# Kernel tuning notes

Measured on AMD Instinct MI355X. Metric: run time of the kernel, lower is better.

Reference implementation:

```python
import jax, jax.numpy as jnp
import numpy as np

B, W, K = 8, 200, 100   # batch, window_size, n_features
KS = 7                   # conv kernel size
HID = 150                # GRU hidden dim
ALPHA = 0.2              # leaky relu slope
FE = 2 * W               # feature GAT embed dim (gatv2 doubles window_size)
TE = 2 * K               # temporal GAT embed dim (gatv2 doubles n_features)


def setup_inputs() -> dict:
    key = jax.random.key(0)
    ks = jax.random.split(key, 16)
    s = lambda k, shape, sc=0.05: jax.random.normal(k, shape, jnp.float32) * sc
    return {
        "x": jax.random.normal(ks[0], (B, W, K), jnp.float32),
        "conv_w": s(ks[1], (K, K, KS)),
        "conv_b": s(ks[2], (K,)),
        "f_lin_w": s(ks[3], (2 * W, FE)),
        "f_lin_b": s(ks[4], (FE,)),
        "f_a": s(ks[5], (FE,)),
        "f_bias": s(ks[6], (K, K)),
        "t_lin_w": s(ks[7], (2 * K, TE)),
        "t_lin_b": s(ks[8], (TE,)),
        "t_a": s(ks[9], (TE,)),
        "t_bias": s(ks[10], (W, W)),
        "w_ih": s(ks[11], (3 * HID, 3 * K)),
        "w_hh": s(ks[12], (3 * HID, HID)),
        "b_ih": s(ks[13], (3 * HID,)),
        "b_hh": s(ks[14], (3 * HID,)),
    }


def _leaky(x):
    return jnp.where(x >= 0, x, ALPHA * x)


def _gatv2(v, lin_w, lin_b, a, bias):
    """GATv2 layer over fully-connected graph. v: (b, N, D).
    e_ij = a . leakyrelu(W [v_i || v_j] + b_lin); out = sigmoid(softmax(e+bias) @ v).
    Splitting W rows avoids materializing the (b,N,N,2D) concat tensor."""
    D = v.shape[-1]
    w1, w2 = lin_w[:D], lin_w[D:]
    si = jnp.einsum('bnd,de->bne', v, w1)  # contribution of node i (repeated)
    sj = jnp.einsum('bnd,de->bne', v, w2)  # contribution of node j (alternating)
    g = _leaky(si[:, :, None, :] + sj[:, None, :, :] + lin_b)  # (b,N,N,E)
    e = jnp.einsum('bije,e->bij', g, a) + bias                 # (b,N,N)
    attn = jax.nn.softmax(e, axis=2)
    return jax.nn.sigmoid(jnp.einsum('bij,bjd->bid', attn, v))  # (b,N,D)


def _forward(x, conv_w, conv_b, f_lin_w, f_lin_b, f_a, f_bias,
             t_lin_w, t_lin_b, t_a, t_bias, w_ih, w_hh, b_ih, b_hh):
    # ConvLayer: permute to (b,K,W), pad 3 both sides, conv1d k=7, relu, permute back
    xc = jnp.transpose(x, (0, 2, 1))
    xc = jax.lax.conv_general_dilated(xc, conv_w, (1,), [((KS - 1) // 2, (KS - 1) // 2)],
                                      dimension_numbers=('NCH', 'OIH', 'NCH'))
    xc = jax.nn.relu(xc + conv_b[None, :, None])
    xc = jnp.transpose(xc, (0, 2, 1))  # (b, W, K)

    # Feature GAT: nodes = features, per-node vector = window
    h_feat = _gatv2(jnp.transpose(xc, (0, 2, 1)), f_lin_w, f_lin_b, f_a, f_bias)
    h_feat = jnp.transpose(h_feat, (0, 2, 1))  # (b, W, K)
    # Temporal GAT: nodes = timesteps, per-node vector = features
    h_temp = _gatv2(xc, t_lin_w, t_lin_b, t_a, t_bias)  # (b, W, K)

    h_cat = jnp.concatenate([xc, h_feat, h_temp], axis=2)  # (b, W, 3K)

    # Single-layer GRU, torch gate order (r, z, n), batch_first; return final hidden
    def step(h, xt):
        gi = xt @ w_ih.T + b_ih
        gh = h @ w_hh.T + b_hh
        ir, iz, inn = jnp.split(gi, 3, axis=-1)
        hr, hz, hn = jnp.split(gh, 3, axis=-1)
        r = jax.nn.sigmoid(ir + hr)
        z = jax.nn.sigmoid(iz + hz)
        n = jnp.tanh(inn + r * hn)
        return (1.0 - z) * n + z * h, None

    h0 = jnp.zeros((x.shape[0], HID), x.dtype)
    h_end, _ = jax.lax.scan(step, h0, jnp.transpose(h_cat, (1, 0, 2)))
    return h_end  # (b, HID)


def reference(x, conv_w, conv_b, f_lin_w, f_lin_b, f_a, f_bias,
              t_lin_w, t_lin_b, t_a, t_bias, w_ih, w_hh, b_ih, b_hh):
    return _forward(x, conv_w, conv_b, f_lin_w, f_lin_b, f_a, f_bias,
                    t_lin_w, t_lin_b, t_a, t_bias, w_ih, w_hh, b_ih, b_hh)
```

## Files before the change

### kernel.cpp

```cpp
#include <hip/hip_runtime.h>
#include <math.h>

#define NB   8
#define NW   200
#define NK   100
#define KSZ  7
#define NHID 150
#define NFE  400
#define NTE  200
#define NG   450
#define NCIN 300
#define ALPHAC 0.2f

typedef __attribute__((ext_vector_type(8))) short bf8;
typedef __attribute__((ext_vector_type(4))) float f32x4;

__device__ __forceinline__ float sigmoidf_(float x){
  return 1.0f/(1.0f + __expf(-x));
}
__device__ __forceinline__ float tanhf_(float x){
  float xc = fminf(fmaxf(x, -15.f), 15.f);
  float e = __expf(2.f*xc);
  return (e - 1.f)/(e + 1.f);
}
__device__ __forceinline__ unsigned short f2bf(float f){
  unsigned int u = __float_as_uint(f);
  unsigned int r = u + 0x7FFFu + ((u>>16)&1u);
  return (unsigned short)(r>>16);
}
__device__ __forceinline__ float lrelu_(float x){
  return fmaxf(x, 0.f) + ALPHAC*fminf(x, 0.f);
}

__global__ void prep_kernel(const float* conv_w, const float* w_ih, const float* w_hh,
                            float* conv_wT, float* w_ihT, unsigned int* Bfrag){
  int idx = blockIdx.x*256 + threadIdx.x;
  const int n1 = NK*NK*KSZ;
  const int n2 = NG*NCIN;
  const int n3 = 32*5*64*4;
  if (idx < n1){
    int k = idx % NK; int it = idx / NK;
    int i = it / KSZ, t = it % KSZ;
    conv_wT[idx] = conv_w[(k*NK + i)*KSZ + t];
  } else if (idx < n1 + n2){
    int o = idx - n1; int g = o % NG; int c = o / NG;
    w_ihT[o] = w_ih[g*NCIN + c];
  } else if (idx < n1 + n2 + n3){
    int o = idx - n1 - n2;
    int n   = o / 1280;
    int rem = o % 1280;
    int ks  = rem / 256;
    int rem2= rem % 256;
    int l   = rem2 >> 2;
    int d   = rem2 & 3;
    int col = n*16 + (l & 15);
    int k0  = ks*32 + (l >> 4)*8 + d*2;
    unsigned short lo = 0, hi = 0;
    if (col < NG){
      if (k0     < NHID) lo = f2bf(w_hh[col*NHID + k0]);
      if (k0 + 1 < NHID) hi = f2bf(w_hh[col*NHID + k0 + 1]);
    }
    Bfrag[o] = ((unsigned int)hi << 16) | lo;
  }
}

__global__ void conv_kernel(const float* x, const float* conv_b, const float* conv_wT, float* xc){
  int idx = blockIdx.x*256 + threadIdx.x;
  if (idx >= NB*NW*NK) return;
  int k = idx % NK; int w = (idx/NK) % NW; int b = idx/(NK*NW);
  float acc = conv_b[k];
  const float* xb = x + b*NW*NK;
  for (int t = 0; t < KSZ; ++t){
    int ws = w + t - 3;
    if (ws < 0 || ws >= NW) continue;
    const float* xr = xb + ws*NK;
    const float* wr = conv_wT + t*NK + k;
    #pragma unroll 4
    for (int i = 0; i < NK; ++i){
      acc += xr[i] * wr[i*KSZ*NK];
    }
  }
  xc[idx] = fmaxf(acc, 0.0f);
}

__global__ void sisj_fused(const float* xc, const float* f_lin_w, float* si_f, float* sj_f,
                           const float* t_lin_w, float* si_t, float* sj_t){
  __shared__ __align__(16) float vt[NW*4];
  int tid = threadIdx.x;
  if (blockIdx.x < 200){
    int b = blockIdx.x / 25; int n0 = (blockIdx.x % 25)*4;
    for (int d = tid; d < NW; d += 512){
      float4 v = *(const float4*)&xc[(b*NW + d)*NK + n0];
      *(float4*)&vt[d*4] = v;
    }
    __syncthreads();
    if (tid >= NFE) return;
    int e = tid;
    float a1[4] = {0,0,0,0}, a2[4] = {0,0,0,0};
    for (int d = 0; d < NW; ++d){
      float w1 = f_lin_w[d*NFE + e];
      float w2 = f_lin_w[(NW + d)*NFE + e];
      float4 v = *(const float4*)&vt[d*4];
      a1[0] += v.x*w1; a1[1] += v.y*w1; a1[2] += v.z*w1; a1[3] += v.w*w1;
      a2[0] += v.x*w2; a2[1] += v.y*w2; a2[2] += v.z*w2; a2[3] += v.w*w2;
    }
    #pragma unroll
    for (int nn = 0; nn < 4; ++nn){
      si_f[(b*NK + n0+nn)*NFE + e] = a1[nn];
      sj_f[(b*NK + n0+nn)*NFE + e] = a2[nn];
    }
  } else {
    int bi = blockIdx.x - 200;
    int b = bi / 50; int n0 = (bi % 50)*4;
    for (int idx = tid; idx < 4*25; idx += 512){
      int nn = idx & 3; int d4 = idx >> 2;
      float4 v = *(const float4*)&xc[(b*NW + n0+nn)*NK + d4*4];
      vt[(d4*4+0)*4 + nn] = v.x;
      vt[(d4*4+1)*4 + nn] = v.y;
      vt[(d4*4+2)*4 + nn] = v.z;
      vt[(d4*4+3)*4 + nn] = v.w;
    }
    __syncthreads();
    if (tid >= NTE) return;
    int e = tid;
    float a1[4] = {0,0,0,0}, a2[4] = {0,0,0,0};
    for (int d = 0; d < NK; ++d){
      float w1 = t_lin_w[d*NTE + e];
      float w2 = t_lin_w[(NK + d)*NTE + e];
      float4 v = *(const float4*)&vt[d*4];
      a1[0] += v.x*w1; a1[1] += v.y*w1; a1[2] += v.z*w1; a1[3] += v.w*w1;
      a2[0] += v.x*w2; a2[1] += v.y*w2; a2[2] += v.z*w2; a2[3] += v.w*w2;
    }
    #pragma unroll
    for (int nn = 0; nn < 4; ++nn){
      si_t[(b*NW + n0+nn)*NTE + e] = a1[nn];
      sj_t[(b*NW + n0+nn)*NTE + e] = a2[nn];
    }
  }
}

__global__ void attn_fused(const float* xc,
                           const float* si_f, const float* sj_f, const float* f_lin_b,
                           const float* f_a, const float* f_bias,
                           const float* si_t, const float* sj_t, const float* t_lin_b,
                           const float* t_a, const float* t_bias,
                           float* h_featT, float* h_temp){
  __shared__ __align__(16) float sib[NFE];
  __shared__ __align__(16) float av[NFE];
  __shared__ __align__(16) float attn[NW];
  __shared__ float red[8];
  int tid = threadIdx.x, lane = tid & 63, wid = tid >> 6;
  if (blockIdx.x < NB*NK){
    int b = blockIdx.x / NK, i = blockIdx.x % NK;
    {
      const float4* si4 = (const float4*)(si_f + (b*NK + i)*NFE);
      const float4* lb4 = (const float4*)f_lin_b;
      const float4* fa4 = (const float4*)f_a;
      for (int e4 = tid; e4 < NFE/4; e4 += 256){
        float4 s = si4[e4], l = lb4[e4];
        float4 o; o.x=s.x+l.x; o.y=s.y+l.y; o.z=s.z+l.z; o.w=s.w+l.w;
        *(float4*)&sib[e4*4] = o;
        *(float4*)&av[e4*4]  = fa4[e4];
      }
    }
    __syncthreads();
    float ej = -1e30f;
    if (tid < NK){
      const float4* sjr4 = (const float4*)(sj_f + (b*NK + tid)*NFE);
      const float4* sib4 = (const float4*)sib;
      const float4* av4  = (const float4*)av;
      float acc = 0.f;
      #pragma unroll 4
      for (int e4 = 0; e4 < NFE/4; ++e4){
        float4 s = sjr4[e4], t = sib4[e4], a = av4[e4];
        acc += a.x*lrelu_(t.x+s.x) + a.y*lrelu_(t.y+s.y)
             + a.z*lrelu_(t.z+s.z) + a.w*lrelu_(t.w+s.w);
      }
      ej = acc + f_bias[i*NK + tid];
    }
    float m = ej;
    #pragma unroll
    for (int off = 32; off > 0; off >>= 1) m = fmaxf(m, __shfl_xor(m, off));
    if (lane == 0) red[wid] = m;
    __syncthreads();
    float bm = fmaxf(fmaxf(red[0], red[1]), fmaxf(red[2], red[3]));
    float ex = (tid < NK) ? __expf(ej - bm) : 0.f;
    float s = ex;
    #pragma unroll
    for (int off = 32; off > 0; off >>= 1) s += __shfl_xor(s, off);
    if (lane == 0) red[4 + wid] = s;
    __syncthreads();
    float denom = red[4] + red[5] + red[6] + red[7];
    if (tid < NK) attn[tid] = ex / denom;
    __syncthreads();
    for (int d = tid; d < NW; d += 256){
      const float4* xr4 = (const float4*)(xc + (b*NW + d)*NK);
      const float4* at4 = (const float4*)attn;
      float acc = 0.f;
      #pragma unroll 5
      for (int j4 = 0; j4 < NK/4; ++j4){
        float4 v = xr4[j4], a = at4[j4];
        acc += a.x*v.x + a.y*v.y + a.z*v.z + a.w*v.w;
      }
      h_featT[(b*NW + d)*NK + i] = sigmoidf_(acc);
    }
  } else {
    int bi = blockIdx.x - NB*NK;
    int b = bi / NW, i = bi % NW;
    {
      const float4* si4 = (const float4*)(si_t + (b*NW + i)*NTE);
      const float4* lb4 = (const float4*)t_lin_b;
      const float4* ta4 = (const float4*)t_a;
      for (int e4 = tid; e4 < NTE/4; e4 += 256){
        float4 s = si4[e4], l = lb4[e4];
        float4 o; o.x=s.x+l.x; o.y=s.y+l.y; o.z=s.z+l.z; o.w=s.w+l.w;
        *(float4*)&sib[e4*4] = o;
        *(float4*)&av[e4*4]  = ta4[e4];
      }
    }
    __syncthreads();
    float ej = -1e30f;
    if (tid < NW){
      const float4* sjr4 = (const float4*)(sj_t + (b*NW + tid)*NTE);
      const float4* sib4 = (const float4*)sib;
      const float4* av4  = (const float4*)av;
      float acc = 0.f;
      #pragma unroll 4
      for (int e4 = 0; e4 < NTE/4; ++e4){
        float4 s = sjr4[e4], t = sib4[e4], a = av4[e4];
        acc += a.x*lrelu_(t.x+s.x) + a.y*lrelu_(t.y+s.y)
             + a.z*lrelu_(t.z+s.z) + a.w*lrelu_(t.w+s.w);
      }
      ej = acc + t_bias[i*NW + tid];
    }
    float m = ej;
    #pragma unroll
    for (int off = 32; off > 0; off >>= 1) m = fmaxf(m, __shfl_xor(m, off));
    if (lane == 0) red[wid] = m;
    __syncthreads();
    float bm = fmaxf(fmaxf(red[0], red[1]), fmaxf(red[2], red[3]));
    float ex = (tid < NW) ? __expf(ej - bm) : 0.f;
    float s = ex;
    #pragma unroll
    for (int off = 32; off > 0; off >>= 1) s += __shfl_xor(s, off);
    if (lane == 0) red[4 + wid] = s;
    __syncthreads();
    float denom = red[4] + red[5] + red[6] + red[7];
    if (tid < NW) attn[tid] = ex / denom;
    __syncthreads();
    for (int d = tid; d < NK; d += 256){
      float acc = 0.f;
      #pragma unroll 4
      for (int j = 0; j < NW; ++j) acc += attn[j]*xc[(b*NW + j)*NK + d];
      h_temp[(b*NW + i)*NK + d] = sigmoidf_(acc);
    }
  }
}

__global__ void gi_kernel(const float* xc, const float* h_featT, const float* h_temp,
                          const float* w_ihT, const float* b_ih, const float* b_hh, float* gi){
  __shared__ __align__(16) float hc[NCIN*8];
  int b = blockIdx.x / 25; int t0 = (blockIdx.x % 25)*8;
  int tid = threadIdx.x;
  for (int idx = tid; idx < NCIN*8; idx += 512){
    int tt = idx / NCIN; int c = idx % NCIN;
    int base = (b*NW + t0 + tt)*NK;
    float v;
    if (c < NK)        v = xc[base + c];
    else if (c < 2*NK) v = h_featT[base + c - NK];
    else               v = h_temp[base + c - 2*NK];
    hc[c*8 + tt] = v;
  }
  __syncthreads();
  if (tid >= NG) return;
  int g = tid;
  float bi = b_ih[g] + ((g < 2*NHID) ? b_hh[g] : 0.f);
  float acc[8];
  #pragma unroll
  for (int tt = 0; tt < 8; ++tt) acc[tt] = bi;
  for (int c = 0; c < NCIN; ++c){
    float wv = w_ihT[c*NG + g];
    float4 h0 = *(const float4*)&hc[c*8];
    float4 h1 = *(const float4*)&hc[c*8+4];
    acc[0] += h0.x*wv; acc[1] += h0.y*wv; acc[2] += h0.z*wv; acc[3] += h0.w*wv;
    acc[4] += h1.x*wv; acc[5] += h1.y*wv; acc[6] += h1.z*wv; acc[7] += h1.w*wv;
  }
  #pragma unroll
  for (int tt = 0; tt < 8; ++tt)
    gi[((t0+tt)*NB + b)*NG + g] = acc[tt];
}

#define STASH(B0,B1,B2,B3, FR) { \
  int4 wq = Bq[(FR)*64 + lane]; \
  asm volatile("v_accvgpr_write_b32 " B0 ", %0\n\t" \
               "v_accvgpr_write_b32 " B1 ", %1\n\t" \
               "v_accvgpr_write_b32 " B2 ", %2\n\t" \
               "v_accvgpr_write_b32 " B3 ", %3" \
               :: "v"(wq.x), "v"(wq.y), "v"(wq.z), "v"(wq.w) \
               : B0, B1, B2, B3); }
#define MMA_INIT(ACC, AF, BR, C0,C1,C2,C3) \
  asm volatile("v_mfma_f32_16x16x32_bf16 %0, %1, " BR ", 0" \
               : "=v"(ACC) : "v"(AF) : C0,C1,C2,C3);
#define MMA_ACC(ACC, AF, BR, C0,C1,C2,C3) \
  asm volatile("v_mfma_f32_16x16x32_bf16 %0, %1, " BR ", %0" \
               : "+v"(ACC) : "v"(AF) : C0,C1,C2,C3);

__device__ __forceinline__ void pack_hilo(float hn, unsigned int& hi2, unsigned int& lo2){
  asm("v_cvt_pk_bf16_f32 %0, %1, %1" : "=v"(hi2) : "v"(hn));
  float hif = __uint_as_float(hi2 << 16);
  float lo = hn - hif;
  asm("v_cvt_pk_bf16_f32 %0, %1, %1" : "=v"(lo2) : "v"(lo));
}

__global__ void __launch_bounds__(768) gru_kernel(const float* gi, const int4* Bq,
                                                  const float* b_hh, float* out){
  __shared__ __align__(16) unsigned short h_bf[16*184];
  __shared__ __align__(16) float gh[512*10];
  int tid = threadIdx.x;
  int lane = tid & 63;
  int wv = tid >> 6;
  int agrp = lane >> 4;
  int arow = lane & 15;

  int b0 = tid/NHID, u0 = tid%NHID;
  bool v1 = (tid < 432);
  int p1 = tid + 768;
  int b1 = v1 ? p1/NHID : 0, u1 = v1 ? p1%NHID : 0;
  float bhn0 = b_hh[2*NHID+u0];
  float bhn1 = b_hh[2*NHID+u1];

  if (wv < 8){
    STASH("a0","a1","a2","a3",     (wv)*5+0)
    STASH("a4","a5","a6","a7",     (wv)*5+1)
    STASH("a8","a9","a10","a11",   (wv)*5+2)
    STASH("a12","a13","a14","a15", (wv)*5+3)
    STASH("a16","a17","a18","a19", (wv)*5+4)
    STASH("a20","a21","a22","a23", (wv+8)*5+0)
    STASH("a24","a25","a26","a27", (wv+8)*5+1)
    STASH("a28","a29","a30","a31", (wv+8)*5+2)
    STASH("a32","a33","a34","a35", (wv+8)*5+3)
    STASH("a36","a37","a38","a39", (wv+8)*5+4)
    STASH("a40","a41","a42","a43", (wv+16)*5+0)
    STASH("a44","a45","a46","a47", (wv+16)*5+1)
    STASH("a48","a49","a50","a51", (wv+16)*5+2)
    STASH("a52","a53","a54","a55", (wv+16)*5+3)
    STASH("a56","a57","a58","a59", (wv+16)*5+4)
    STASH("a60","a61","a62","a63", (wv+24)*5+0)
    STASH("a64","a65","a66","a67", (wv+24)*5+1)
    STASH("a68","a69","a70","a71", (wv+24)*5+2)
    STASH("a72","a73","a74","a75", (wv+24)*5+3)
    STASH("a76","a77","a78","a79", (wv+24)*5+4)
  }

  for (int i = tid; i < 16*184; i += 768) h_bf[i] = 0;
  __syncthreads();

  const bf8* HB = (const bf8*)h_bf;
  int abase = arow*23 + agrp;

  float hold0 = 0.f, hold1 = 0.f;

  const float* gp0 = gi + b0*NG + u0;
  const float* gp1 = gi + b1*NG + u1;
  float cr0 = gp0[0], cz0 = gp0[NHID], cn0 = gp0[2*NHID];
  float cr1 = 0.f, cz1 = 0.f, cn1 = 0.f;
  if (v1){ cr1 = gp1[0]; cz1 = gp1[NHID]; cn1 = gp1[2*NHID]; }

  const float* ghp0 = &gh[u0*10 + b0];
  const float* ghp1 = &gh[u1*10 + b1];
  unsigned short* hb0h = &h_bf[(2*b0)*184 + u0];
  unsigned short* hb0l = &h_bf[(2*b0+1)*184 + u0];
  unsigned short* hb1h = &h_bf[(2*b1)*184 + u1];
  unsigned short* hb1l = &h_bf[(2*b1+1)*184 + u1];

  for (int t = 0; t < NW; ++t){
    gp0 += NB*NG; gp1 += NB*NG;
    float nr0 = gp0[0], nz0 = gp0[NHID], nn0 = gp0[2*NHID];
    float nr1 = 0.f, nz1 = 0.f, nn1 = 0.f;
    if (v1){ nr1 = gp1[0]; nz1 = gp1[NHID]; nn1 = gp1[2*NHID]; }

    if (wv < 8){
      bf8 A0 = HB[abase],    A1 = HB[abase+4],  A2 = HB[abase+8],
          A3 = HB[abase+12], A4 = HB[abase+16];
      f32x4 c0, c1, c2, c3;
      MMA_INIT(c0, A0, "a[0:3]",   "a0","a1","a2","a3")
      MMA_INIT(c1, A0, "a[20:23]", "a20","a21","a22","a23")
      MMA_INIT(c2, A0, "a[40:43]", "a40","a41","a42","a43")
      MMA_INIT(c3, A0, "a[60:63]", "a60","a61","a62","a63")
      MMA_ACC (c0, A1, "a[4:7]",   "a4","a5","a6","a7")
      MMA_ACC (c1, A1, "a[24:27]", "a24","a25","a26","a27")
      MMA_ACC (c2, A1, "a[44:47]", "a44","a45","a46","a47")
      MMA_ACC (c3, A1, "a[64:67]", "a64","a65","a66","a67")
      MMA_ACC (c0, A2, "a[8:11]",  "a8","a9","a10","a11")
      MMA_ACC (c1, A2, "a[28:31]", "a28","a29","a30","a31")
      MMA_ACC (c2, A2, "a[48:51]", "a48","a49","a50","a51")
      MMA_ACC (c3, A2, "a[68:71]", "a68","a69","a70","a71")
      MMA_ACC (c0, A3, "a[12:15]", "a12","a13","a14","a15")
      MMA_ACC (c1, A3, "a[32:35]", "a32","a33","a34","a35")
      MMA_ACC (c2, A3, "a[52:55]", "a52","a53","a54","a55")
      MMA_ACC (c3, A3, "a[72:75]", "a72","a73","a74","a75")
      MMA_ACC (c0, A4, "a[16:19]", "a16","a17","a18","a19")
      MMA_ACC (c1, A4, "a[36:39]", "a36","a37","a38","a39")
      MMA_ACC (c2, A4, "a[56:59]", "a56","a57","a58","a59")
      MMA_ACC (c3, A4, "a[76:79]", "a76","a77","a78","a79")
      asm volatile("s_nop 7\n\ts_nop 7" ::: );

      int cb = agrp*2;
      float2 s0, s1, s2, s3;
      s0.x = c0[0]+c0[1]; s0.y = c0[2]+c0[3];
      s1.x = c1[0]+c1[1]; s1.y = c1[2]+c1[3];
      s2.x = c2[0]+c2[1]; s2.y = c2[2]+c2[3];
      s3.x = c3[0]+c3[1]; s3.y = c3[2]+c3[3];
      *(float2*)&gh[((wv    )*16 + arow)*10 + cb] = s0;
      *(float2*)&gh[((wv+ 8)*16 + arow)*10 + cb] = s1;
      *(float2*)&gh[((wv+16)*16 + arow)*10 + cb] = s2;
      *(float2*)&gh[((wv+24)*16 + arow)*10 + cb] = s3;
    }
    __syncthreads();

    {
      float r = sigmoidf_(cr0 + ghp0[0]);
      float z = sigmoidf_(cz0 + ghp0[NHID*10]);
      float n = tanhf_  (cn0 + r*(ghp0[2*NHID*10] + bhn0));
      float hn = (1.f - z)*n + z*hold0;
      hold0 = hn;
      unsigned int hi2, lo2;
      pack_hilo(hn, hi2, lo2);
      *hb0h = (unsigned short)hi2;
      *hb0l = (unsigned short)lo2;
    }
    if (v1){
      float r = sigmoidf_(cr1 + ghp1[0]);
      float z = sigmoidf_(cz1 + ghp1[NHID*10]);
      float n = tanhf_  (cn1 + r*(ghp1[2*NHID*10] + bhn1));
      float hn = (1.f - z)*n + z*hold1;
      hold1 = hn;
      unsigned int hi2, lo2;
      pack_hilo(hn, hi2, lo2);
      *hb1h = (unsigned short)hi2;
      *hb1l = (unsigned short)lo2;
    }
    __syncthreads();

    cr0 = nr0; cz0 = nz0; cn0 = nn0;
    cr1 = nr1; cz1 = nz1; cn1 = nn1;
  }

  out[b0*NHID + u0] = hold0;
  if (v1) out[b1*NHID + u1] = hold1;
}

extern "C" void kernel_launch(void* const* d_in, const int* in_sizes, int n_in,
                              void* d_out, int out_size, void* d_ws, size_t ws_size,
                              hipStream_t stream){
  const float* x       = (const float*)d_in[0];
  const float* conv_w  = (const float*)d_in[1];
  const float* conv_b  = (const float*)d_in[2];
  const float* f_lin_w = (const float*)d_in[3];
  const float* f_lin_b = (const float*)d_in[4];
  const float* f_a     = (const float*)d_in[5];
  const float* f_bias  = (const float*)d_in[6];
  const float* t_lin_w = (const float*)d_in[7];
  const float* t_lin_b = (const float*)d_in[8];
  const float* t_a     = (const float*)d_in[9];
  const float* t_bias  = (const float*)d_in[10];
  const float* w_ih    = (const float*)d_in[11];
  const float* w_hh    = (const float*)d_in[12];
  const float* b_ih    = (const float*)d_in[13];
  const float* b_hh    = (const float*)d_in[14];

  float* ws      = (float*)d_ws;
  float* xc      = ws;
  float* conv_wT = ws + 160000;
  float* si_f    = ws + 230000;
  float* sj_f    = ws + 550000;
  float* h_featT = ws + 870000;
  float* si_t    = ws + 1030000;
  float* sj_t    = ws + 1350000;
  float* h_temp  = ws + 1670000;
  float* w_ihT   = ws + 1830000;
  float* gi      = ws + 1965000;
  float* BfragF  = ws + 2685000;

  prep_kernel<<<961, 256, 0, stream>>>(conv_w, w_ih, w_hh, conv_wT, w_ihT, (unsigned int*)BfragF);
  conv_kernel<<<(NB*NW*NK + 255)/256, 256, 0, stream>>>(x, conv_b, conv_wT, xc);
  sisj_fused<<<600, 512, 0, stream>>>(xc, f_lin_w, si_f, sj_f, t_lin_w, si_t, sj_t);
  attn_fused<<<2400, 256, 0, stream>>>(xc, si_f, sj_f, f_lin_b, f_a, f_bias,
                                       si_t, sj_t, t_lin_b, t_a, t_bias, h_featT, h_temp);
  gi_kernel<<<200, 512, 0, stream>>>(xc, h_featT, h_temp, w_ihT, b_ih, b_hh, gi);
  gru_kernel<<<1, 768, 0, stream>>>(gi, (const int4*)BfragF, b_hh, (float*)d_out);
}
```

Measured before the change: 398.9 us.

## Restructure GRU recurrence so MFMA output lands in gate-owning lanes

```diff
diff --git a/kernel.cpp b/kernel.cpp
--- a/kernel.cpp
+++ b/kernel.cpp
@@ -47,16 +47,27 @@
     w_ihT[o] = w_ih[g*NCIN + c];
   } else if (idx < n1 + n2 + n3){
     int o = idx - n1 - n2;
-    int n   = o / 1280;
-    int rem = o % 1280;
-    int ks  = rem / 256;
-    int rem2= rem % 256;
-    int l   = rem2 >> 2;
-    int d   = rem2 & 3;
-    int col = n*16 + (l & 15);
-    int k0  = ks*32 + (l >> 4)*8 + d*2;
+    int ntile = o / 1280;
+    int rem  = o % 1280;
+    int ks   = rem / 256;
+    int rem2 = rem % 256;
+    int l    = rem2 >> 2;
+    int d    = rem2 & 3;
+    int w    = ntile & 7;
+    int tidx = ntile >> 3;
+    int m    = l & 15;
+    int gm   = m >> 2;
+    int r    = m & 3;
+    int p    = r*4 + tidx;
+    int col  = -1;
+    if (p < 15){
+      int q = p/3, gam = p%3;
+      int s = w*20 + gm*5 + q;
+      if (s < NHID) col = gam*NHID + s;
+    }
+    int k0 = ks*32 + (l >> 4)*8 + d*2;
     unsigned short lo = 0, hi = 0;
-    if (col < NG){
+    if (col >= 0){
       if (k0     < NHID) lo = f2bf(w_hh[col*NHID + k0]);
       if (k0 + 1 < NHID) hi = f2bf(w_hh[col*NHID + k0 + 1]);
     }
@@ -258,7 +269,7 @@
 }
 
 __global__ void gi_kernel(const float* xc, const float* h_featT, const float* h_temp,
-                          const float* w_ihT, const float* b_ih, const float* b_hh, float* gi){
+                          const float* w_ihT, const float* b_ih, const float* b_hh, float* gi_p){
   __shared__ __align__(16) float hc[NCIN*8];
   int b = blockIdx.x / 25; int t0 = (blockIdx.x % 25)*8;
   int tid = threadIdx.x;
@@ -285,9 +296,11 @@
     acc[0] += h0.x*wv; acc[1] += h0.y*wv; acc[2] += h0.z*wv; acc[3] += h0.w*wv;
     acc[4] += h1.x*wv; acc[5] += h1.y*wv; acc[6] += h1.z*wv; acc[7] += h1.w*wv;
   }
+  int gam = (g < NHID) ? 0 : ((g < 2*NHID) ? 1 : 2);
+  int u = g - gam*NHID;
   #pragma unroll
   for (int tt = 0; tt < 8; ++tt)
-    gi[((t0+tt)*NB + b)*NG + g] = acc[tt];
+    gi_p[(((t0+tt)*160 + u)*3 + gam)*8 + b] = acc[tt];
 }
 
 #define STASH(B0,B1,B2,B3, FR) { \
@@ -298,12 +311,12 @@
                "v_accvgpr_write_b32 " B3 ", %3" \
                :: "v"(wq.x), "v"(wq.y), "v"(wq.z), "v"(wq.w) \
                : B0, B1, B2, B3); }
-#define MMA_INIT(ACC, AF, BR, C0,C1,C2,C3) \
-  asm volatile("v_mfma_f32_16x16x32_bf16 %0, %1, " BR ", 0" \
-               : "=v"(ACC) : "v"(AF) : C0,C1,C2,C3);
-#define MMA_ACC(ACC, AF, BR, C0,C1,C2,C3) \
-  asm volatile("v_mfma_f32_16x16x32_bf16 %0, %1, " BR ", %0" \
-               : "+v"(ACC) : "v"(AF) : C0,C1,C2,C3);
+#define MMA_INIT(ACC, AR, BF, C0,C1,C2,C3) \
+  asm volatile("v_mfma_f32_16x16x32_bf16 %0, " AR ", %1, 0" \
+               : "=v"(ACC) : "v"(BF) : C0,C1,C2,C3);
+#define MMA_ACC(ACC, AR, BF, C0,C1,C2,C3) \
+  asm volatile("v_mfma_f32_16x16x32_bf16 %0, " AR ", %1, %0" \
+               : "+v"(ACC) : "v"(BF) : C0,C1,C2,C3);
 
 __device__ __forceinline__ void pack_hilo(float hn, unsigned int& hi2, unsigned int& lo2){
   asm("v_cvt_pk_bf16_f32 %0, %1, %1" : "=v"(hi2) : "v"(hn));
@@ -312,142 +325,162 @@
   asm("v_cvt_pk_bf16_f32 %0, %1, %1" : "=v"(lo2) : "v"(lo));
 }
 
-__global__ void __launch_bounds__(768) gru_kernel(const float* gi, const int4* Bq,
+__global__ void __launch_bounds__(512) gru_kernel(const float* gi_p, const int4* Bq,
                                                   const float* b_hh, float* out){
-  __shared__ __align__(16) unsigned short h_bf[16*184];
-  __shared__ __align__(16) float gh[512*10];
+  __shared__ __align__(16) unsigned short h_b0[16*168];
+  __shared__ __align__(16) unsigned short h_b1[16*168];
   int tid = threadIdx.x;
   int lane = tid & 63;
   int wv = tid >> 6;
-  int agrp = lane >> 4;
-  int arow = lane & 15;
-
-  int b0 = tid/NHID, u0 = tid%NHID;
-  bool v1 = (tid < 432);
-  int p1 = tid + 768;
-  int b1 = v1 ? p1/NHID : 0, u1 = v1 ? p1%NHID : 0;
-  float bhn0 = b_hh[2*NHID+u0];
-  float bhn1 = b_hh[2*NHID+u1];
-
-  if (wv < 8){
-    STASH("a0","a1","a2","a3",     (wv)*5+0)
-    STASH("a4","a5","a6","a7",     (wv)*5+1)
-    STASH("a8","a9","a10","a11",   (wv)*5+2)
-    STASH("a12","a13","a14","a15", (wv)*5+3)
-    STASH("a16","a17","a18","a19", (wv)*5+4)
-    STASH("a20","a21","a22","a23", (wv+8)*5+0)
-    STASH("a24","a25","a26","a27", (wv+8)*5+1)
-    STASH("a28","a29","a30","a31", (wv+8)*5+2)
-    STASH("a32","a33","a34","a35", (wv+8)*5+3)
-    STASH("a36","a37","a38","a39", (wv+8)*5+4)
-    STASH("a40","a41","a42","a43", (wv+16)*5+0)
-    STASH("a44","a45","a46","a47", (wv+16)*5+1)
-    STASH("a48","a49","a50","a51", (wv+16)*5+2)
-    STASH("a52","a53","a54","a55", (wv+16)*5+3)
-    STASH("a56","a57","a58","a59", (wv+16)*5+4)
-    STASH("a60","a61","a62","a63", (wv+24)*5+0)
-    STASH("a64","a65","a66","a67", (wv+24)*5+1)
-    STASH("a68","a69","a70","a71", (wv+24)*5+2)
-    STASH("a72","a73","a74","a75", (wv+24)*5+3)
-    STASH("a76","a77","a78","a79", (wv+24)*5+4)
-  }
-
-  for (int i = tid; i < 16*184; i += 768) h_bf[i] = 0;
+  int g  = lane >> 4;
+  int n  = lane & 15;
+  int b  = n >> 1;
+  int P  = n & 1;
+
+  int s0 = wv*20 + g*5 + (P ? 3 : 0);
+  int s1 = s0 + 1;
+  int s2 = s0 + 2;
+  bool v0 = (s0 < NHID);
+  bool v1 = (s1 < NHID);
+  bool v2 = (P == 0) && (s2 < NHID);
+
+  float bhn0 = b_hh[2*NHID + (v0 ? s0 : 0)];
+  float bhn1 = b_hh[2*NHID + (v1 ? s1 : 0)];
+  float bhn2 = b_hh[2*NHID + (v2 ? s2 : 0)];
+
+  STASH("a0","a1","a2","a3",     (wv)*5+0)
+  STASH("a4","a5","a6","a7",     (wv)*5+1)
+  STASH("a8","a9","a10","a11",   (wv)*5+2)
+  STASH("a12","a13","a14","a15", (wv)*5+3)
+  STASH("a16","a17","a18","a19", (wv)*5+4)
+  STASH("a20","a21","a22","a23", (wv+8)*5+0)
+  STASH("a24","a25","a26","a27", (wv+8)*5+1)
+  STASH("a28","a29","a30","a31", (wv+8)*5+2)
+  STASH("a32","a33","a34","a35", (wv+8)*5+3)
+  STASH("a36","a37","a38","a39", (wv+8)*5+4)
+  STASH("a40","a41","a42","a43", (wv+16)*5+0)
+  STASH("a44","a45","a46","a47", (wv+16)*5+1)
+  STASH("a48","a49","a50","a51", (wv+16)*5+2)
+  STASH("a52","a53","a54","a55", (wv+16)*5+3)
+  STASH("a56","a57","a58","a59", (wv+16)*5+4)
+  STASH("a60","a61","a62","a63", (wv+24)*5+0)
+  STASH("a64","a65","a66","a67", (wv+24)*5+1)
+  STASH("a68","a69","a70","a71", (wv+24)*5+2)
+  STASH("a72","a73","a74","a75", (wv+24)*5+3)
+  STASH("a76","a77","a78","a79", (wv+24)*5+4)
+
+  for (int i = tid; i < 16*168; i += 512){ h_b0[i] = 0; h_b1[i] = 0; }
   __syncthreads();
 
-  const bf8* HB = (const bf8*)h_bf;
-  int abase = arow*23 + agrp;
-
-  float hold0 = 0.f, hold1 = 0.f;
-
-  const float* gp0 = gi + b0*NG + u0;
-  const float* gp1 = gi + b1*NG + u1;
-  float cr0 = gp0[0], cz0 = gp0[NHID], cn0 = gp0[2*NHID];
-  float cr1 = 0.f, cz1 = 0.f, cn1 = 0.f;
-  if (v1){ cr1 = gp1[0]; cz1 = gp1[NHID]; cn1 = gp1[2*NHID]; }
-
-  const float* ghp0 = &gh[u0*10 + b0];
-  const float* ghp1 = &gh[u1*10 + b1];
-  unsigned short* hb0h = &h_bf[(2*b0)*184 + u0];
-  unsigned short* hb0l = &h_bf[(2*b0+1)*184 + u0];
-  unsigned short* hb1h = &h_bf[(2*b1)*184 + u1];
-  unsigned short* hb1l = &h_bf[(2*b1+1)*184 + u1];
+  int rb_base = n*21 + g;
+
+  int wa0h = (2*b)*168   + (s0>>3)*8 + (s0&7);
+  int wa0l = wa0h + 168;
+  int wa1h = (2*b)*168   + (s1>>3)*8 + (s1&7);
+  int wa1l = wa1h + 168;
+  int wa2h = (2*b)*168   + (s2>>3)*8 + (s2&7);
+  int wa2l = wa2h + 168;
+
+  float hold0 = 0.f, hold1 = 0.f, hold2 = 0.f;
+
+  const float* gp = gi_p + (s0*3)*8 + b;
+  float cr0 = gp[0],  cz0 = gp[8],  cn0 = gp[16];
+  float cr1 = gp[24], cz1 = gp[32], cn1 = gp[40];
+  float cr2 = gp[48], cz2 = gp[56], cn2 = gp[64];
 
   for (int t = 0; t < NW; ++t){
-    gp0 += NB*NG; gp1 += NB*NG;
-    float nr0 = gp0[0], nz0 = gp0[NHID], nn0 = gp0[2*NHID];
-    float nr1 = 0.f, nz1 = 0.f, nn1 = 0.f;
-    if (v1){ nr1 = gp1[0]; nz1 = gp1[NHID]; nn1 = gp1[2*NHID]; }
-
-    if (wv < 8){
-      bf8 A0 = HB[abase],    A1 = HB[abase+4],  A2 = HB[abase+8],
-          A3 = HB[abase+12], A4 = HB[abase+16];
-      f32x4 c0, c1, c2, c3;
-      MMA_INIT(c0, A0, "a[0:3]",   "a0","a1","a2","a3")
-      MMA_INIT(c1, A0, "a[20:23]", "a20","a21","a22","a23")
-      MMA_INIT(c2, A0, "a[40:43]", "a40","a41","a42","a43")
-      MMA_INIT(c3, A0, "a[60:63]", "a60","a61","a62","a63")
-      MMA_ACC (c0, A1, "a[4:7]",   "a4","a5","a6","a7")
-      MMA_ACC (c1, A1, "a[24:27]", "a24","a25","a26","a27")
-      MMA_ACC (c2, A1, "a[44:47]", "a44","a45","a46","a47")
-      MMA_ACC (c3, A1, "a[64:67]", "a64","a65","a66","a67")
-      MMA_ACC (c0, A2, "a[8:11]",  "a8","a9","a10","a11")
-      MMA_ACC (c1, A2, "a[28:31]", "a28","a29","a30","a31")
-      MMA_ACC (c2, A2, "a[48:51]", "a48","a49","a50","a51")
-      MMA_ACC (c3, A2, "a[68:71]", "a68","a69","a70","a71")
-      MMA_ACC (c0, A3, "a[12:15]", "a12","a13","a14","a15")
-      MMA_ACC (c1, A3, "a[32:35]", "a32","a33","a34","a35")
-      MMA_ACC (c2, A3, "a[52:55]", "a52","a53","a54","a55")
-      MMA_ACC (c3, A3, "a[72:75]", "a72","a73","a74","a75")
-      MMA_ACC (c0, A4, "a[16:19]", "a16","a17","a18","a19")
-      MMA_ACC (c1, A4, "a[36:39]", "a36","a37","a38","a39")
-      MMA_ACC (c2, A4, "a[56:59]", "a56","a57","a58","a59")
-      MMA_ACC (c3, A4, "a[76:79]", "a76","a77","a78","a79")
-      asm volatile("s_nop 7\n\ts_nop 7" ::: );
-
-      int cb = agrp*2;
-      float2 s0, s1, s2, s3;
-      s0.x = c0[0]+c0[1]; s0.y = c0[2]+c0[3];
-      s1.x = c1[0]+c1[1]; s1.y = c1[2]+c1[3];
-      s2.x = c2[0]+c2[1]; s2.y = c2[2]+c2[3];
-      s3.x = c3[0]+c3[1]; s3.y = c3[2]+c3[3];
-      *(float2*)&gh[((wv    )*16 + arow)*10 + cb] = s0;
-      *(float2*)&gh[((wv+ 8)*16 + arow)*10 + cb] = s1;
-      *(float2*)&gh[((wv+16)*16 + arow)*10 + cb] = s2;
-      *(float2*)&gh[((wv+24)*16 + arow)*10 + cb] = s3;
-    }
-    __syncthreads();
+    const unsigned short* rbuf = (t & 1) ? h_b1 : h_b0;
+    unsigned short*       wbuf = (t & 1) ? h_b0 : h_b1;
+
+    gp += 160*3*8;
+    float nr0 = gp[0],  nz0 = gp[8],  nn0 = gp[16];
+    float nr1 = gp[24], nz1 = gp[32], nn1 = gp[40];
+    float nr2 = gp[48], nz2 = gp[56], nn2 = gp[64];
+
+    const bf8* HB = (const bf8*)rbuf;
+    bf8 B0 = HB[rb_base],    B1 = HB[rb_base+4],  B2 = HB[rb_base+8],
+        B3 = HB[rb_base+12], B4 = HB[rb_base+16];
+
+    f32x4 c0, c1, c2, c3;
+    MMA_INIT(c0, "a[0:3]",   B0, "a0","a1","a2","a3")
+    MMA_INIT(c1, "a[20:23]", B0, "a20","a21","a22","a23")
+    MMA_INIT(c2, "a[40:43]", B0, "a40","a41","a42","a43")
+    MMA_INIT(c3, "a[60:63]", B0, "a60","a61","a62","a63")
+    MMA_ACC (c0, "a[4:7]",   B1, "a4","a5","a6","a7")
+    MMA_ACC (c1, "a[24:27]", B1, "a24","a25","a26","a27")
+    MMA_ACC (c2, "a[44:47]", B1, "a44","a45","a46","a47")
+    MMA_ACC (c3, "a[64:67]", B1, "a64","a65","a66","a67")
+    MMA_ACC (c0, "a[8:11]",  B2, "a8","a9","a10","a11")
+    MMA_ACC (c1, "a[28:31]", B2, "a28","a29","a30","a31")
+    MMA_ACC (c2, "a[48:51]", B2, "a48","a49","a50","a51")
+    MMA_ACC (c3, "a[68:71]", B2, "a68","a69","a70","a71")
+    MMA_ACC (c0, "a[12:15]", B3, "a12","a13","a14","a15")
+    MMA_ACC (c1, "a[32:35]", B3, "a32","a33","a34","a35")
+    MMA_ACC (c2, "a[52:55]", B3, "a52","a53","a54","a55")
+    MMA_ACC (c3, "a[72:75]", B3, "a72","a73","a74","a75")
+    MMA_ACC (c0, "a[16:19]", B4, "a16","a17","a18","a19")
+    MMA_ACC (c1, "a[36:39]", B4, "a36","a37","a38","a39")
+    MMA_ACC (c2, "a[56:59]", B4, "a56","a57","a58","a59")
+    MMA_ACC (c3, "a[76:79]", B4, "a76","a77","a78","a79")
+    asm volatile("s_nop 7\n\ts_nop 7" ::: );
+
+    float f00=c0[0]; f00 += __shfl_xor(f00,1);
+    float f10=c1[0]; f10 += __shfl_xor(f10,1);
+    float f20=c2[0]; f20 += __shfl_xor(f20,1);
+    float f30=c3[0]; f30 += __shfl_xor(f30,1);
+    float f01=c0[1]; f01 += __shfl_xor(f01,1);
+    float f11=c1[1]; f11 += __shfl_xor(f11,1);
+    float f21=c2[1]; f21 += __shfl_xor(f21,1);
+    float f31=c3[1]; f31 += __shfl_xor(f31,1);
+    float f02=c0[2]; f02 += __shfl_xor(f02,1);
+    float f12=c1[2]; f12 += __shfl_xor(f12,1);
+    float f22=c2[2]; f22 += __shfl_xor(f22,1);
+    float f32=c3[2]; f32 += __shfl_xor(f32,1);
+    float f03=c0[3]; f03 += __shfl_xor(f03,1);
+    float f13=c1[3]; f13 += __shfl_xor(f13,1);
+    float f23=c2[3]; f23 += __shfl_xor(f23,1);
+
+    float ghr0 = P ? f12 : f00, ghz0 = P ? f22 : f10, ghn0 = P ? f32 : f20;
+    float ghr1 = P ? f03 : f30, ghz1 = P ? f13 : f01, ghn1 = P ? f23 : f11;
+    float ghr2 = f21,           ghz2 = f31,           ghn2 = f02;
 
     {
-      float r = sigmoidf_(cr0 + ghp0[0]);
-      float z = sigmoidf_(cz0 + ghp0[NHID*10]);
-      float n = tanhf_  (cn0 + r*(ghp0[2*NHID*10] + bhn0));
-      float hn = (1.f - z)*n + z*hold0;
+      float r = sigmoidf_(cr0 + ghr0);
+      float z = sigmoidf_(cz0 + ghz0);
+      float nn = tanhf_ (cn0 + r*(ghn0 + bhn0));
+      float hn = (1.f - z)*nn + z*hold0;
       hold0 = hn;
-      unsigned int hi2, lo2;
-      pack_hilo(hn, hi2, lo2);
-      *hb0h = (unsigned short)hi2;
-      *hb0l = (unsigned short)lo2;
-    }
-    if (v1){
-      float r = sigmoidf_(cr1 + ghp1[0]);
-      float z = sigmoidf_(cz1 + ghp1[NHID*10]);
-      float n = tanhf_  (cn1 + r*(ghp1[2*NHID*10] + bhn1));
-      float hn = (1.f - z)*n + z*hold1;
+      if (v0){ unsigned int h2,l2; pack_hilo(hn,h2,l2);
+               wbuf[wa0h]=(unsigned short)h2; wbuf[wa0l]=(unsigned short)l2; }
+    }
+    {
+      float r = sigmoidf_(cr1 + ghr1);
+      float z = sigmoidf_(cz1 + ghz1);
+      float nn = tanhf_ (cn1 + r*(ghn1 + bhn1));
+      float hn = (1.f - z)*nn + z*hold1;
       hold1 = hn;
-      unsigned int hi2, lo2;
-      pack_hilo(hn, hi2, lo2);
-      *hb1h = (unsigned short)hi2;
-      *hb1l = (unsigned short)lo2;
+      if (v1){ unsigned int h2,l2; pack_hilo(hn,h2,l2);
+               wbuf[wa1h]=(unsigned short)h2; wbuf[wa1l]=(unsigned short)l2; }
+    }
+    {
+      float r = sigmoidf_(cr2 + ghr2);
+      float z = sigmoidf_(cz2 + ghz2);
+      float nn = tanhf_ (cn2 + r*(ghn2 + bhn2));
+      float hn = (1.f - z)*nn + z*hold2;
+      hold2 = hn;
+      if (v2){ unsigned int h2,l2; pack_hilo(hn,h2,l2);
+               wbuf[wa2h]=(unsigned short)h2; wbuf[wa2l]=(unsigned short)l2; }
     }
     __syncthreads();
 
     cr0 = nr0; cz0 = nz0; cn0 = nn0;
     cr1 = nr1; cz1 = nz1; cn1 = nn1;
-  }
-
-  out[b0*NHID + u0] = hold0;
-  if (v1) out[b1*NHID + u1] = hold1;
+    cr2 = nr2; cz2 = nz2; cn2 = nn2;
+  }
+
+  if (v0) out[b*NHID + s0] = hold0;
+  if (v1) out[b*NHID + s1] = hold1;
+  if (v2) out[b*NHID + s2] = hold2;
 }
 
 extern "C" void kernel_launch(void* const* d_in, const int* in_sizes, int n_in,
@@ -479,14 +512,14 @@
   float* sj_t    = ws + 1350000;
   float* h_temp  = ws + 1670000;
   float* w_ihT   = ws + 1830000;
-  float* gi      = ws + 1965000;
-  float* BfragF  = ws + 2685000;
+  float* gi_p    = ws + 1965000;
+  float* BfragF  = ws + 2733000;
 
   prep_kernel<<<961, 256, 0, stream>>>(conv_w, w_ih, w_hh, conv_wT, w_ihT, (unsigned int*)BfragF);
   conv_kernel<<<(NB*NW*NK + 255)/256, 256, 0, stream>>>(x, conv_b, conv_wT, xc);
   sisj_fused<<<600, 512, 0, stream>>>(xc, f_lin_w, si_f, sj_f, t_lin_w, si_t, sj_t);
   attn_fused<<<2400, 256, 0, stream>>>(xc, si_f, sj_f, f_lin_b, f_a, f_bias,
                                        si_t, sj_t, t_lin_b, t_a, t_bias, h_featT, h_temp);
-  gi_kernel<<<200, 512, 0, stream>>>(xc, h_featT, h_temp, w_ihT, b_ih, b_hh, gi);
-  gru_kernel<<<1, 768, 0, stream>>>(gi, (const int4*)BfragF, b_hh, (float*)d_out);
-}
+  gi_kernel<<<200, 512, 0, stream>>>(xc, h_featT, h_temp, w_ihT, b_ih, b_hh, gi_p);
+  gru_kernel<<<1, 512, 0, stream>>>(gi_p, (const int4*)BfragF, b_hh, (float*)d_out);
+}
```

After: 455.6 us. 14.2% more time.
